# Kernel tuning notes

Measured on AMD Instinct MI355X. Metric: run time of the kernel, lower is better.

The kernel has to match this reference:

```python
import jax, jax.numpy as jnp
import numpy as np

B, P, E, D, A, M, V, T = 64, 196, 2048, 512, 512, 512, 10000, 31


def setup_inputs() -> dict:
    key = jax.random.key(0)
    ks = jax.random.split(key, 20)
    s = 0.02
    inp = {
        "encoder_out": jax.random.normal(ks[0], (B, P, E), jnp.float32),
        "captions": jax.random.randint(ks[1], (B, T), 0, V),
        "caption_lengths": jax.random.randint(ks[2], (B,), 2, T + 1).at[0].set(T),
        # parameters
        "W_emb": jax.random.normal(ks[3], (V, M), jnp.float32) * s,
        "We": jax.random.normal(ks[4], (A, E), jnp.float32) * s,
        "be": jnp.zeros((A,), jnp.float32),
        "Wd": jax.random.normal(ks[5], (A, D), jnp.float32) * s,
        "bd": jnp.zeros((A,), jnp.float32),
        "wf": jax.random.normal(ks[6], (1, A), jnp.float32) * s,
        "bf": jnp.zeros((1,), jnp.float32),
        "Wih": jax.random.normal(ks[7], (4 * D, M + E), jnp.float32) * s,
        "bih": jnp.zeros((4 * D,), jnp.float32),
        "Whh": jax.random.normal(ks[8], (4 * D, D), jnp.float32) * s,
        "bhh": jnp.zeros((4 * D,), jnp.float32),
        "Wfc": jax.random.normal(ks[9], (V, D), jnp.float32) * s,
        "bfc": jnp.zeros((V,), jnp.float32),
        "Wh0": jax.random.normal(ks[10], (D, E), jnp.float32) * s,
        "bh0": jnp.zeros((D,), jnp.float32),
        "Wc0": jax.random.normal(ks[11], (D, E), jnp.float32) * s,
        "bc0": jnp.zeros((D,), jnp.float32),
    }
    return inp


def _decode(encoder_out, W_emb, We, be, Wd, bd, wf, bf, Wih, bih, Whh, bhh,
            Wfc, bfc, Wh0, bh0, Wc0, bc0, captions, caption_lengths):
    # sort by length descending (matches torch .sort(descending=True))
    idx = jnp.argsort(-caption_lengths)
    lens = caption_lengths[idx]
    enc = encoder_out[idx]              # [B,P,E]
    caps = captions[idx]                # [B,T]
    emb = W_emb[caps]                   # [B,T,M]
    mean_enc = enc.mean(axis=1)         # [B,E]
    h0 = mean_enc @ Wh0.T + bh0         # [B,D]
    c0 = mean_enc @ Wc0.T + bc0
    dec_len = lens - 1                  # [B]
    att1 = enc @ We.T + be              # [B,P,A] precomputed encoder projection
    Tmax = caps.shape[1] - 1

    def step(carry, xs):
        h, c = carry
        e_t, t = xs                     # e_t: [B,M]
        active = (t < dec_len)          # [B]
        att2 = h @ Wd.T + bd            # [B,A]
        scores = jnp.tanh(att1 + att2[:, None, :]) @ wf[0] + bf[0]  # [B,P]
        alpha = jax.nn.softmax(scores, axis=-1)                      # [B,P]
        ctx = jnp.einsum('bp,bpe->be', alpha, enc)                   # [B,E]
        x = jnp.concatenate([e_t, ctx], axis=-1)                     # [B,M+E]
        gates = x @ Wih.T + bih + h @ Whh.T + bhh                    # [B,4D]
        i_g, f_g, g_g, o_g = jnp.split(gates, 4, axis=-1)
        c_t = jax.nn.sigmoid(f_g) * c + jax.nn.sigmoid(i_g) * jnp.tanh(g_g)
        h_t = jax.nn.sigmoid(o_g) * jnp.tanh(c_t)
        pred = h_t @ Wfc.T + bfc        # dropout in eval mode = identity
        m = active[:, None]
        h_new = jnp.where(m, h_t, h)
        c_new = jnp.where(m, c_t, c)
        pred = jnp.where(m, pred, 0.0)
        alpha = jnp.where(m, alpha, 0.0)
        return (h_new, c_new), (pred, alpha)

    emb_ts = jnp.swapaxes(emb[:, :Tmax, :], 0, 1)  # [Tmax,B,M]
    ts = jnp.arange(Tmax)
    _, (preds, alphas) = jax.lax.scan(step, (h0, c0), (emb_ts, ts))
    predictions = jnp.swapaxes(preds, 0, 1)   # [B,Tmax,V]
    alphas = jnp.swapaxes(alphas, 0, 1)       # [B,Tmax,P]
    return predictions, alphas


def reference(encoder_out, captions, caption_lengths, W_emb, We, be, Wd, bd,
              wf, bf, Wih, bih, Whh, bhh, Wfc, bfc, Wh0, bh0, Wc0, bc0):
    return _decode(encoder_out, W_emb, We, be, Wd, bd, wf, bf, Wih, bih,
                   Whh, bhh, Wfc, bfc, Wh0, bh0, Wc0, bc0,
                   captions, caption_lengths)
```

## Files before the change

kernel.cpp:

```cpp
#include <hip/hip_runtime.h>
#include <cstdint>
#include <cstddef>

typedef __attribute__((ext_vector_type(8))) short short8;
typedef __attribute__((ext_vector_type(4))) float f32x4;

#define DEV static __device__ __forceinline__

#define PRED_ELEMS 19200000ULL

#define OFF_ENC   0ULL
#define OFF_ATT1  51380224ULL
#define OFF_B1    64225280ULL
#define OFF_WFC   69468160ULL
#define OFF_WEB   79724544ULL
#define OFF_B0    81821696ULL
#define OFF_B2    86016000ULL
#define OFF_MEAN  94404608ULL
#define OFF_HX    94666752ULL
#define OFF_C     94797824ULL
#define OFF_ATT2  94928896ULL
#define OFF_GEH   95059968ULL
#define OFF_CTX   95584256ULL
#define OFF_SC    95846400ULL
#define OFF_META  95896576ULL

DEV float b2f(unsigned short u){ unsigned v = ((unsigned)u) << 16; float f; __builtin_memcpy(&f, &v, 4); return f; }
DEV unsigned short f2b(float x){ unsigned v; __builtin_memcpy(&v, &x, 4); unsigned r = v + 0x7fffu + ((v >> 16) & 1u); return (unsigned short)(r >> 16); }
DEV float sigm(float x){ return 1.0f / (1.0f + __expf(-x)); }

DEV void gload16(const void* g, void* l){
  __builtin_amdgcn_global_load_lds((const __attribute__((address_space(1))) unsigned int*)g,
                                   (__attribute__((address_space(3))) unsigned int*)l, 16, 0, 0);
}

DEV void mm_core(const unsigned short* A, int ldA, int m0,
                 const unsigned short* Bm, int ldB, int n0,
                 int kIters, unsigned short* As, unsigned short* Bs, f32x4 acc[4])
{
  const int tid = threadIdx.x;
  const int lane = tid & 63, w = tid >> 6;
  const unsigned short* ga = A + (size_t)(m0 + lane) * ldA + w * 8;
  const unsigned short* gb = Bm + (size_t)(n0 + lane) * ldB + w * 8;
  unsigned short* la = As + w * 512;
  unsigned short* lb = Bs + w * 512;
  const int kb = lane >> 4, rr = lane & 15;
  for (int kk = 0; kk < kIters; ++kk) {
    gload16(ga, la); gload16(gb, lb);
    ga += 32; gb += 32;
    asm volatile("s_waitcnt vmcnt(0)" ::: "memory");
    __syncthreads();
    short8 bfr = *(const short8*)(Bs + (size_t)(kb * 64 + w * 16 + rr) * 8);
#pragma unroll
    for (int f = 0; f < 4; ++f) {
      short8 afr = *(const short8*)(As + (size_t)(kb * 64 + f * 16 + rr) * 8);
      acc[f] = __builtin_amdgcn_mfma_f32_16x16x32_bf16(afr, bfr, acc[f], 0, 0, 0);
    }
    __syncthreads();
  }
}

__global__ void k_meta(const int* __restrict__ caps, const int* __restrict__ lens, int* __restrict__ meta){
  int j = threadIdx.x;
  int lj = lens[j];
  int rank = 0;
  for (int k = 0; k < 64; ++k) { int lk = lens[k]; rank += (lk > lj) || (lk == lj && k < j); }
  meta[rank] = j; meta[64 + rank] = lj - 1;
  for (int t = 0; t < 31; ++t) meta[160 + rank * 31 + t] = caps[j * 31 + t];
  __syncthreads();
  if (j < 30) { int c = 0; for (int b = 0; b < 64; ++b) c += (meta[64 + b] > j); meta[128 + j] = c; }
}

__global__ __launch_bounds__(256) void k_encg(const float* __restrict__ enc, const int* __restrict__ meta, unsigned short* __restrict__ encb){
  int row = blockIdx.x; int b = row / 196, p = row % 196;
  const float* src = enc + ((size_t)meta[b] * 196 + p) * 2048;
  unsigned short* dst = encb + (size_t)row * 2048;
  int e0 = threadIdx.x * 8;
  short8 o;
#pragma unroll
  for (int j = 0; j < 8; ++j) o[j] = (short)f2b(src[e0 + j]);
  *(short8*)(dst + e0) = o;
}

__global__ __launch_bounds__(256) void k_wconv(const float* We, const float* Wh0, const float* Wc0,
                        const float* Wd, const float* Whh, const float* Wih, const float* Wfc,
                        unsigned short* Web, unsigned short* B0, unsigned short* B1,
                        unsigned short* Wfcb, unsigned short* B2){
  int bid = blockIdx.x, tid = threadIdx.x;
  if (bid < 512) {
    const float* s = We + (size_t)bid * 2048; unsigned short* d = Web + (size_t)bid * 2048;
    int e0 = tid * 8; short8 o;
#pragma unroll
    for (int j = 0; j < 8; ++j) o[j] = (short)f2b(s[e0 + j]);
    *(short8*)(d + e0) = o;
  } else if (bid < 1536) {
    int r = bid - 512;
    const float* s = (r < 512) ? (Wh0 + (size_t)r * 2048) : (Wc0 + (size_t)(r - 512) * 2048);
    unsigned short* d = B0 + (size_t)r * 2048;
    int e0 = tid * 8; short8 o;
#pragma unroll
    for (int j = 0; j < 8; ++j) o[j] = (short)f2b(s[e0 + j]);
    *(short8*)(d + e0) = o;
  } else if (bid < 3584) {
    int jr = bid - 1536; int g = (jr & 3) * 512 + (jr >> 2);
    const float* s = Wih + (size_t)g * 2560 + 512;
    unsigned short* d = B2 + (size_t)jr * 2048;
    int e0 = tid * 8; short8 o;
#pragma unroll
    for (int j = 0; j < 8; ++j) o[j] = (short)f2b(s[e0 + j]);
    *(short8*)(d + e0) = o;
  } else if (bid < 6144) {
    int n = bid - 3584; unsigned short* d = B1 + (size_t)n * 1024;
    int k0 = tid * 4;
    if (n < 512) {
#pragma unroll
      for (int j = 0; j < 4; ++j) { int k = k0 + j; d[k] = (k < 512) ? f2b(Wd[(size_t)n * 512 + k]) : (unsigned short)0; }
    } else {
      int j2 = n - 512; int g = (j2 & 3) * 512 + (j2 >> 2);
#pragma unroll
      for (int j = 0; j < 4; ++j) { int k = k0 + j;
        d[k] = (k < 512) ? f2b(Whh[(size_t)g * 512 + k]) : f2b(Wih[(size_t)g * 2560 + (k - 512)]); }
    }
  } else {
    int v = bid - 6144; unsigned short* d = Wfcb + (size_t)v * 512;
    int k0 = tid * 2;
#pragma unroll
    for (int j = 0; j < 2; ++j) d[k0 + j] = (v < 10000) ? f2b(Wfc[(size_t)v * 512 + k0 + j]) : (unsigned short)0;
  }
}

__global__ __launch_bounds__(256) void k_mean(const unsigned short* __restrict__ encb, unsigned short* __restrict__ meanb){
  int b = blockIdx.y, ch = blockIdx.x;
  int e = ch * 512 + threadIdx.x * 2;
  const unsigned short* ep = encb + (size_t)b * 196 * 2048 + e;
  float s0 = 0.f, s1 = 0.f;
  for (int p = 0; p < 196; ++p) {
    unsigned u = *(const unsigned*)(ep + (size_t)p * 2048);
    s0 += b2f((unsigned short)(u & 0xffff));
    s1 += b2f((unsigned short)(u >> 16));
  }
  const float inv = 1.0f / 196.0f;
  unsigned o = ((unsigned)f2b(s1 * inv) << 16) | f2b(s0 * inv);
  *(unsigned*)(meanb + (size_t)b * 2048 + e) = o;
}

__global__ __launch_bounds__(256) void k_h0c0(const unsigned short* meanb, const unsigned short* B0,
                      const float* bh0, const float* bc0, unsigned short* hx, float* cbuf){
  __shared__ __align__(16) unsigned short As[2048], Bs[2048];
  f32x4 acc[4];
#pragma unroll
  for (int f = 0; f < 4; ++f) acc[f] = (f32x4){0.f,0.f,0.f,0.f};
  int nt = blockIdx.x;
  mm_core(meanb, 2048, 0, B0, 2048, nt * 64, 64, As, Bs, acc);
  int lane = threadIdx.x & 63, w = threadIdx.x >> 6;
  int col = lane & 15, rhi = lane >> 4;
  int n = nt * 64 + w * 16 + col;
#pragma unroll
  for (int f = 0; f < 4; ++f)
#pragma unroll
    for (int r = 0; r < 4; ++r) {
      int b = f * 16 + rhi * 4 + r; float v = acc[f][r];
      if (n < 512) hx[(size_t)b * 1024 + n] = f2b(v + bh0[n]);
      else cbuf[(size_t)b * 512 + (n - 512)] = v + bc0[n - 512];
    }
}

__global__ void k_emb0(const float* __restrict__ Wemb, const int* __restrict__ meta, unsigned short* __restrict__ hx){
  int b = blockIdx.x;
  int cap = meta[160 + b * 31];
  for (int j = threadIdx.x; j < 512; j += 256)
    hx[(size_t)b * 1024 + 512 + j] = f2b(Wemb[(size_t)cap * 512 + j]);
}

__global__ __launch_bounds__(256) void k_att1(const unsigned short* __restrict__ encb,
                      const unsigned short* __restrict__ Web,
                      const float* __restrict__ be, unsigned short* __restrict__ att1b){
  __shared__ __align__(16) unsigned short As[4096];
  int tid = threadIdx.x, w = tid >> 6, lane = tid & 63;
  int mt = blockIdx.x;
  int rr = lane & 15, kb8 = (lane >> 4) * 8;
  f32x4 acc[4][8];
#pragma unroll
  for (int f = 0; f < 4; ++f)
#pragma unroll
    for (int q = 0; q < 8; ++q) acc[f][q] = (f32x4){0.f,0.f,0.f,0.f};

  const unsigned short* ga = encb + (size_t)(mt * 64 + lane) * 2048 + w * 8;
  gload16(ga, As + w * 512);
  asm volatile("s_waitcnt vmcnt(0)" ::: "memory");
  __syncthreads();
  int cb = 0;
  for (int kk = 0; kk < 64; ++kk) {
    int nb = cb ^ 1;
    if (kk < 63) gload16(ga + (kk + 1) * 32, As + (nb << 11) + w * 512);
    short8 af[4];
#pragma unroll
    for (int f = 0; f < 4; ++f)
      af[f] = *(const short8*)(As + (cb << 11) + ((size_t)((lane >> 4) * 64 + f * 16 + rr)) * 8);
#pragma unroll
    for (int q = 0; q < 8; ++q) {
      short8 bfr = *(const short8*)(Web + (size_t)(w * 128 + q * 16 + rr) * 2048 + kk * 32 + kb8);
#pragma unroll
      for (int f = 0; f < 4; ++f)
        acc[f][q] = __builtin_amdgcn_mfma_f32_16x16x32_bf16(af[f], bfr, acc[f][q], 0, 0, 0);
    }
    asm volatile("s_waitcnt vmcnt(0)" ::: "memory");
    __syncthreads();
    cb ^= 1;
  }
  int col = lane & 15, rhi = lane >> 4;
  float bev[8];
#pragma unroll
  for (int q = 0; q < 8; ++q) bev[q] = be[w * 128 + q * 16 + col];
#pragma unroll
  for (int f = 0; f < 4; ++f)
#pragma unroll
    for (int r = 0; r < 4; ++r) {
      int m = mt * 64 + f * 16 + rhi * 4 + r;
#pragma unroll
      for (int q = 0; q < 8; ++q)
        att1b[(size_t)m * 512 + w * 128 + q * 16 + col] = f2b(acc[f][q][r] + bev[q]);
    }
}

__global__ __launch_bounds__(256) void k_step1(int t, const unsigned short* __restrict__ hx,
                       const unsigned short* __restrict__ B1, const unsigned short* __restrict__ Wfcb,
                       const float* __restrict__ bd, const float* __restrict__ bih, const float* __restrict__ bhh,
                       const float* __restrict__ bfc, const int* __restrict__ meta,
                       float* __restrict__ att2f, float* __restrict__ geh, float* __restrict__ out){
  int w = threadIdx.x >> 6, lane = threadIdx.x & 63;
  int omega = blockIdx.x * 4 + w;
  if (omega >= 786) return;
  int rr = lane & 15, kb8 = (lane >> 4) * 8;
  const unsigned short* pb; int kIt;
  if (omega < 32)       { if (t == 30) return; pb = B1 + (size_t)(omega * 16 + rr) * 1024 + kb8; kIt = 16; }
  else if (omega < 160) { if (t == 30) return; pb = B1 + (size_t)(512 + (omega - 32) * 16 + rr) * 1024 + kb8; kIt = 32; }
  else                  { if (t == 0)  return; pb = Wfcb + (size_t)((omega - 160) * 16 + rr) * 512 + kb8; kIt = 16; }
  const unsigned short* pa0 = hx + (size_t)rr * 1024 + kb8;
  f32x4 acc[4];
#pragma unroll
  for (int f = 0; f < 4; ++f) acc[f] = (f32x4){0.f,0.f,0.f,0.f};
#pragma unroll 4
  for (int kk = 0; kk < kIt; ++kk) {
    short8 bfr = *(const short8*)(pb + kk * 32);
#pragma unroll
    for (int f = 0; f < 4; ++f) {
      short8 afr = *(const short8*)(pa0 + (size_t)f * 16384 + kk * 32);
      acc[f] = __builtin_amdgcn_mfma_f32_16x16x32_bf16(afr, bfr, acc[f], 0, 0, 0);
    }
  }
  int col = lane & 15, rhi = lane >> 4;
  if (omega < 32) {
    int n = omega * 16 + col; float bv = bd[n];
#pragma unroll
    for (int f = 0; f < 4; ++f)
#pragma unroll
      for (int r = 0; r < 4; ++r) { int b = f * 16 + rhi * 4 + r; att2f[(size_t)b * 512 + n] = acc[f][r] + bv; }
  } else if (omega < 160) {
    int j = (omega - 32) * 16 + col; int g = (j & 3) * 512 + (j >> 2);
    float bv = bih[g] + bhh[g];
#pragma unroll
    for (int f = 0; f < 4; ++f)
#pragma unroll
      for (int r = 0; r < 4; ++r) { int b = f * 16 + rhi * 4 + r; geh[(size_t)b * 2048 + j] = acc[f][r] + bv; }
  } else {
    int v = (omega - 160) * 16 + col;
    if (v < 10000) {
      int na = meta[128 + t - 1];
      float bv = bfc[v];
#pragma unroll
      for (int f = 0; f < 4; ++f)
#pragma unroll
        for (int r = 0; r < 4; ++r) {
          int b = f * 16 + rhi * 4 + r;
          if (b < na) out[(size_t)b * 300000 + (size_t)(t - 1) * 10000 + v] = acc[f][r] + bv;
        }
    }
  }
}

__global__ __launch_bounds__(256) void k_scores(int t, const unsigned short* __restrict__ att1b, const float* __restrict__ att2f,
                        const float* __restrict__ wf, const float* __restrict__ bfp,
                        const int* __restrict__ meta, float* __restrict__ sc){
  int b = blockIdx.y, pc = blockIdx.x;
  if (b >= meta[128 + t]) return;
  int tid = threadIdx.x, lane = tid & 63, w = tid >> 6;
  float wfr[8], a2[8];
#pragma unroll
  for (int j = 0; j < 8; ++j) { wfr[j] = wf[lane * 8 + j]; a2[j] = att2f[(size_t)b * 512 + lane * 8 + j]; }
  float bf0 = bfp[0];
  for (int pi = w; pi < 49; pi += 4) {
    int p = pc * 49 + pi;
    short8 av = *(const short8*)(att1b + ((size_t)(b * 196 + p)) * 512 + lane * 8);
    float s = 0.f;
#pragma unroll
    for (int j = 0; j < 8; ++j) s += tanhf(b2f((unsigned short)av[j]) + a2[j]) * wfr[j];
#pragma unroll
    for (int off = 32; off; off >>= 1) s += __shfl_xor(s, off);
    if (lane == 0) sc[(size_t)b * 196 + p] = s + bf0;
  }
}

__global__ __launch_bounds__(256) void k_ctx(int t, const float* __restrict__ sc, const unsigned short* __restrict__ encb,
                     const int* __restrict__ meta, float* __restrict__ out, unsigned short* __restrict__ ctxb){
  int b = blockIdx.y, ch = blockIdx.x;
  if (b >= meta[128 + t]) return;
  int tid = threadIdx.x;
  __shared__ float red[256];
  __shared__ float sal[200];
  __shared__ float part[4][512];
  float v = (tid < 196) ? sc[(size_t)b * 196 + tid] : -3.0e38f;
  red[tid] = v; __syncthreads();
  for (int s = 128; s; s >>= 1) { if (tid < s) red[tid] = fmaxf(red[tid], red[tid + s]); __syncthreads(); }
  float mx = red[0]; __syncthreads();
  float ex = (tid < 196) ? __expf(v - mx) : 0.f;
  red[tid] = ex; __syncthreads();
  for (int s = 128; s; s >>= 1) { if (tid < s) red[tid] += red[tid + s]; __syncthreads(); }
  float inv = 1.0f / red[0];
  if (tid < 196) {
    float al = ex * inv;
    sal[tid] = al;
    if (ch == 0) out[PRED_ELEMS + ((size_t)b * 30 + t) * 196 + tid] = al;
  }
  __syncthreads();
  int w = tid >> 6, lane = tid & 63;
  const unsigned short* ep = encb + (size_t)b * 196 * 2048 + ch * 512 + lane * 8;
  float s[8];
#pragma unroll
  for (int j = 0; j < 8; ++j) s[j] = 0.f;
#pragma unroll 7
  for (int i = 0; i < 49; ++i) {
    int p = w + i * 4;
    short8 vv = *(const short8*)(ep + (size_t)p * 2048);
    float a = sal[p];
#pragma unroll
    for (int j = 0; j < 8; ++j) s[j] += a * b2f((unsigned short)vv[j]);
  }
#pragma unroll
  for (int j = 0; j < 8; ++j) part[w][lane * 8 + j] = s[j];
  __syncthreads();
  float r0 = part[0][tid * 2] + part[1][tid * 2] + part[2][tid * 2] + part[3][tid * 2];
  float r1 = part[0][tid * 2 + 1] + part[1][tid * 2 + 1] + part[2][tid * 2 + 1] + part[3][tid * 2 + 1];
  unsigned o = ((unsigned)f2b(r1) << 16) | f2b(r0);
  *(unsigned*)(ctxb + (size_t)b * 2048 + ch * 512 + tid * 2) = o;
}

__global__ __launch_bounds__(256) void k_step2(int t, const unsigned short* __restrict__ ctxb,
                       const unsigned short* __restrict__ B2, const float* __restrict__ geh,
                       const float* __restrict__ Wemb, const int* __restrict__ meta,
                       float* __restrict__ cbuf, unsigned short* __restrict__ hx){
  __shared__ float red[4][64][17];
  int w = threadIdx.x >> 6, lane = threadIdx.x & 63;
  int n0 = blockIdx.x * 16;
  int rr = lane & 15, kb8 = (lane >> 4) * 8;
  const unsigned short* pb = B2 + (size_t)(n0 + rr) * 2048 + w * 512 + kb8;
  const unsigned short* pa0 = ctxb + (size_t)rr * 2048 + w * 512 + kb8;
  f32x4 acc[4];
#pragma unroll
  for (int f = 0; f < 4; ++f) acc[f] = (f32x4){0.f,0.f,0.f,0.f};
#pragma unroll 4
  for (int kk = 0; kk < 16; ++kk) {
    short8 bfr = *(const short8*)(pb + kk * 32);
#pragma unroll
    for (int f = 0; f < 4; ++f) {
      short8 afr = *(const short8*)(pa0 + (size_t)f * 32768 + kk * 32);
      acc[f] = __builtin_amdgcn_mfma_f32_16x16x32_bf16(afr, bfr, acc[f], 0, 0, 0);
    }
  }
  int col = lane & 15, rhi = lane >> 4;
#pragma unroll
  for (int f = 0; f < 4; ++f)
#pragma unroll
    for (int r = 0; r < 4; ++r) red[w][f * 16 + rhi * 4 + r][col] = acc[f][r];
  __syncthreads();
  int b = threadIdx.x >> 2, dl = threadIdx.x & 3;
  int d = (n0 >> 2) + dl;
  float g4[4];
#pragma unroll
  for (int q = 0; q < 4; ++q) {
    int nl = dl * 4 + q;
    g4[q] = red[0][b][nl] + red[1][b][nl] + red[2][b][nl] + red[3][b][nl]
          + geh[(size_t)b * 2048 + n0 + nl];
  }
  float c0 = cbuf[(size_t)b * 512 + d];
  float ct = sigm(g4[1]) * c0 + sigm(g4[0]) * tanhf(g4[2]);
  float ht = sigm(g4[3]) * tanhf(ct);
  int na = meta[128 + t];
  if (b < na) { cbuf[(size_t)b * 512 + d] = ct; hx[(size_t)b * 1024 + d] = f2b(ht); }
  int cap = meta[160 + b * 31 + t + 1];
  hx[(size_t)b * 1024 + 512 + d] = f2b(Wemb[(size_t)cap * 512 + d]);
}

extern "C" void kernel_launch(void* const* d_in, const int* in_sizes, int n_in,
                              void* d_out, int out_size, void* d_ws, size_t ws_size,
                              hipStream_t stream) {
  (void)in_sizes; (void)n_in; (void)ws_size;
  const float* enc  = (const float*)d_in[0];
  const int*   caps = (const int*)d_in[1];
  const int*   lens = (const int*)d_in[2];
  const float* Wemb = (const float*)d_in[3];
  const float* We   = (const float*)d_in[4];
  const float* be   = (const float*)d_in[5];
  const float* Wd   = (const float*)d_in[6];
  const float* bd   = (const float*)d_in[7];
  const float* wf   = (const float*)d_in[8];
  const float* bf   = (const float*)d_in[9];
  const float* Wih  = (const float*)d_in[10];
  const float* bih  = (const float*)d_in[11];
  const float* Whh  = (const float*)d_in[12];
  const float* bhh  = (const float*)d_in[13];
  const float* Wfc  = (const float*)d_in[14];
  const float* bfc  = (const float*)d_in[15];
  const float* Wh0  = (const float*)d_in[16];
  const float* bh0  = (const float*)d_in[17];
  const float* Wc0  = (const float*)d_in[18];
  const float* bc0  = (const float*)d_in[19];

  char* ws = (char*)d_ws;
  unsigned short* encb  = (unsigned short*)(ws + OFF_ENC);
  unsigned short* att1b = (unsigned short*)(ws + OFF_ATT1);
  unsigned short* B1    = (unsigned short*)(ws + OFF_B1);
  unsigned short* Wfcb  = (unsigned short*)(ws + OFF_WFC);
  unsigned short* Web   = (unsigned short*)(ws + OFF_WEB);
  unsigned short* B0    = (unsigned short*)(ws + OFF_B0);
  unsigned short* B2    = (unsigned short*)(ws + OFF_B2);
  unsigned short* meanb = (unsigned short*)(ws + OFF_MEAN);
  unsigned short* hx    = (unsigned short*)(ws + OFF_HX);
  float*          cbuf  = (float*)(ws + OFF_C);
  float*          att2f = (float*)(ws + OFF_ATT2);
  float*          geh   = (float*)(ws + OFF_GEH);
  unsigned short* ctxb  = (unsigned short*)(ws + OFF_CTX);
  float*          sc    = (float*)(ws + OFF_SC);
  int*            meta  = (int*)(ws + OFF_META);
  float* out = (float*)d_out;

  hipMemsetAsync(d_out, 0, (size_t)out_size * sizeof(float), stream);
  k_meta<<<1, 64, 0, stream>>>(caps, lens, meta);
  k_encg<<<12544, 256, 0, stream>>>(enc, meta, encb);
  k_wconv<<<16160, 256, 0, stream>>>(We, Wh0, Wc0, Wd, Whh, Wih, Wfc, Web, B0, B1, Wfcb, B2);
  k_mean<<<dim3(4, 64), 256, 0, stream>>>(encb, meanb);
  k_h0c0<<<16, 256, 0, stream>>>(meanb, B0, bh0, bc0, hx, cbuf);
  k_emb0<<<64, 256, 0, stream>>>(Wemb, meta, hx);
  k_att1<<<196, 256, 0, stream>>>(encb, Web, be, att1b);
  for (int t = 0; t <= 30; ++t) {
    k_step1<<<197, 256, 0, stream>>>(t, hx, B1, Wfcb, bd, bih, bhh, bfc, meta, att2f, geh, out);
    if (t < 30) {
      k_scores<<<dim3(4, 64), 256, 0, stream>>>(t, att1b, att2f, wf, bf, meta, sc);
      k_ctx<<<dim3(4, 64), 256, 0, stream>>>(t, sc, encb, meta, out, ctxb);
      k_step2<<<128, 256, 0, stream>>>(t, ctxb, B2, geh, Wemb, meta, cbuf, hx);
    }
  }
}
```

Measured before the change: 2.012 ms.

## Defer vocab projection to one batched GEMM and fuse attention scoring per step

The per-step output projection onto the vocabulary is taken out of the recurrent loop. Hidden states are collected into a buffer, and a single tiled GEMM (k_pred) computes all predictions at the end. The att2 projection, scores and softmax are merged into one per-batch kernel. The Whh gate term moves into the LSTM-cell kernel, and the hidden/input buffer is ping-ponged, which removes k_step1 and one launch per step. k_att1 is retiled to 128x128 with LDS double buffering for both operands, and tanh is replaced by an exp-based approximation. The risks are the reduced accuracy of the tanh approximation and the hh buffer aliasing the B0 region, which appears safe because B0 is only read by k_h0c0 before the loop.

```diff
diff --git a/kernel.cpp b/kernel.cpp
--- a/kernel.cpp
+++ b/kernel.cpp
@@ -15,19 +15,19 @@
 #define OFF_WFC   69468160ULL
 #define OFF_WEB   79724544ULL
 #define OFF_B0    81821696ULL
+#define OFF_HH    81821696ULL
 #define OFF_B2    86016000ULL
-#define OFF_MEAN  94404608ULL
-#define OFF_HX    94666752ULL
-#define OFF_C     94797824ULL
-#define OFF_ATT2  94928896ULL
-#define OFF_GEH   95059968ULL
-#define OFF_CTX   95584256ULL
-#define OFF_SC    95846400ULL
-#define OFF_META  95896576ULL
+#define OFF_HX0   94404608ULL
+#define OFF_HX1   94535680ULL
+#define OFF_C     94666752ULL
+#define OFF_SC    94797824ULL
+#define OFF_CTX   94848000ULL
+#define OFF_META  95110144ULL
 
 DEV float b2f(unsigned short u){ unsigned v = ((unsigned)u) << 16; float f; __builtin_memcpy(&f, &v, 4); return f; }
 DEV unsigned short f2b(float x){ unsigned v; __builtin_memcpy(&v, &x, 4); unsigned r = v + 0x7fffu + ((v >> 16) & 1u); return (unsigned short)(r >> 16); }
 DEV float sigm(float x){ return 1.0f / (1.0f + __expf(-x)); }
+DEV float tanhf_fast(float x){ float e = __expf(2.0f * x); return 1.0f - 2.0f / (e + 1.0f); }
 
 DEV void gload16(const void* g, void* l){
   __builtin_amdgcn_global_load_lds((const __attribute__((address_space(1))) unsigned int*)g,
@@ -175,141 +175,113 @@
 __global__ __launch_bounds__(256) void k_att1(const unsigned short* __restrict__ encb,
                       const unsigned short* __restrict__ Web,
                       const float* __restrict__ be, unsigned short* __restrict__ att1b){
-  __shared__ __align__(16) unsigned short As[4096];
-  int tid = threadIdx.x, w = tid >> 6, lane = tid & 63;
-  int mt = blockIdx.x;
-  int rr = lane & 15, kb8 = (lane >> 4) * 8;
-  f32x4 acc[4][8];
+  __shared__ __align__(16) unsigned short As[2][4096], Bs[2][4096];
+  int tid = threadIdx.x, lane = tid & 63, w = tid >> 6;
+  int mt = blockIdx.x >> 2, nt = blockIdx.x & 3;
+  int wr = (w >> 1) * 64, wc = (w & 1) * 64;
+  int rr = lane & 15, kb = lane >> 4;
+  f32x4 acc[4][4];
 #pragma unroll
   for (int f = 0; f < 4; ++f)
 #pragma unroll
-    for (int q = 0; q < 8; ++q) acc[f][q] = (f32x4){0.f,0.f,0.f,0.f};
-
-  const unsigned short* ga = encb + (size_t)(mt * 64 + lane) * 2048 + w * 8;
-  gload16(ga, As + w * 512);
-  asm volatile("s_waitcnt vmcnt(0)" ::: "memory");
-  __syncthreads();
-  int cb = 0;
+    for (int q = 0; q < 4; ++q) acc[f][q] = (f32x4){0.f,0.f,0.f,0.f};
+
+  const unsigned short* gA = encb + (size_t)mt * 128 * 2048;
+  const unsigned short* gB = Web + (size_t)nt * 128 * 2048;
+  int L0 = tid, L1 = tid + 256;
+  size_t s0 = (size_t)(L0 & 127) * 2048 + ((L0 >> 7) << 3);
+  size_t s1 = (size_t)(L1 & 127) * 2048 + ((L1 >> 7) << 3);
+  int d0 = (w * 64) * 8, d1 = (w * 64 + 256) * 8;
+
+#define STAGE_A1(kk, bf) do { \
+    gload16(gA + s0 + (size_t)(kk) * 32, &As[bf][d0]); \
+    gload16(gB + s0 + (size_t)(kk) * 32, &Bs[bf][d0]); \
+    gload16(gA + s1 + (size_t)(kk) * 32, &As[bf][d1]); \
+    gload16(gB + s1 + (size_t)(kk) * 32, &Bs[bf][d1]); \
+  } while (0)
+
+  STAGE_A1(0, 0);
+  __syncthreads();
   for (int kk = 0; kk < 64; ++kk) {
-    int nb = cb ^ 1;
-    if (kk < 63) gload16(ga + (kk + 1) * 32, As + (nb << 11) + w * 512);
-    short8 af[4];
+    int cur = kk & 1;
+    if (kk < 63) STAGE_A1(kk + 1, cur ^ 1);
+    short8 af[4], bq[4];
 #pragma unroll
     for (int f = 0; f < 4; ++f)
-      af[f] = *(const short8*)(As + (cb << 11) + ((size_t)((lane >> 4) * 64 + f * 16 + rr)) * 8);
-#pragma unroll
-    for (int q = 0; q < 8; ++q) {
-      short8 bfr = *(const short8*)(Web + (size_t)(w * 128 + q * 16 + rr) * 2048 + kk * 32 + kb8);
-#pragma unroll
-      for (int f = 0; f < 4; ++f)
-        acc[f][q] = __builtin_amdgcn_mfma_f32_16x16x32_bf16(af[f], bfr, acc[f][q], 0, 0, 0);
-    }
-    asm volatile("s_waitcnt vmcnt(0)" ::: "memory");
+      af[f] = *(const short8*)&As[cur][((kb << 7) + wr + f * 16 + rr) * 8];
+#pragma unroll
+    for (int q = 0; q < 4; ++q)
+      bq[q] = *(const short8*)&Bs[cur][((kb << 7) + wc + q * 16 + rr) * 8];
+#pragma unroll
+    for (int f = 0; f < 4; ++f)
+#pragma unroll
+      for (int q = 0; q < 4; ++q)
+        acc[f][q] = __builtin_amdgcn_mfma_f32_16x16x32_bf16(af[f], bq[q], acc[f][q], 0, 0, 0);
     __syncthreads();
-    cb ^= 1;
-  }
+  }
+#undef STAGE_A1
   int col = lane & 15, rhi = lane >> 4;
-  float bev[8];
-#pragma unroll
-  for (int q = 0; q < 8; ++q) bev[q] = be[w * 128 + q * 16 + col];
-#pragma unroll
-  for (int f = 0; f < 4; ++f)
-#pragma unroll
-    for (int r = 0; r < 4; ++r) {
-      int m = mt * 64 + f * 16 + rhi * 4 + r;
-#pragma unroll
-      for (int q = 0; q < 8; ++q)
-        att1b[(size_t)m * 512 + w * 128 + q * 16 + col] = f2b(acc[f][q][r] + bev[q]);
-    }
-}
-
-__global__ __launch_bounds__(256) void k_step1(int t, const unsigned short* __restrict__ hx,
-                       const unsigned short* __restrict__ B1, const unsigned short* __restrict__ Wfcb,
-                       const float* __restrict__ bd, const float* __restrict__ bih, const float* __restrict__ bhh,
-                       const float* __restrict__ bfc, const int* __restrict__ meta,
-                       float* __restrict__ att2f, float* __restrict__ geh, float* __restrict__ out){
-  int w = threadIdx.x >> 6, lane = threadIdx.x & 63;
-  int omega = blockIdx.x * 4 + w;
-  if (omega >= 786) return;
-  int rr = lane & 15, kb8 = (lane >> 4) * 8;
-  const unsigned short* pb; int kIt;
-  if (omega < 32)       { if (t == 30) return; pb = B1 + (size_t)(omega * 16 + rr) * 1024 + kb8; kIt = 16; }
-  else if (omega < 160) { if (t == 30) return; pb = B1 + (size_t)(512 + (omega - 32) * 16 + rr) * 1024 + kb8; kIt = 32; }
-  else                  { if (t == 0)  return; pb = Wfcb + (size_t)((omega - 160) * 16 + rr) * 512 + kb8; kIt = 16; }
-  const unsigned short* pa0 = hx + (size_t)rr * 1024 + kb8;
-  f32x4 acc[4];
-#pragma unroll
-  for (int f = 0; f < 4; ++f) acc[f] = (f32x4){0.f,0.f,0.f,0.f};
-#pragma unroll 4
-  for (int kk = 0; kk < kIt; ++kk) {
-    short8 bfr = *(const short8*)(pb + kk * 32);
-#pragma unroll
-    for (int f = 0; f < 4; ++f) {
-      short8 afr = *(const short8*)(pa0 + (size_t)f * 16384 + kk * 32);
-      acc[f] = __builtin_amdgcn_mfma_f32_16x16x32_bf16(afr, bfr, acc[f], 0, 0, 0);
-    }
-  }
-  int col = lane & 15, rhi = lane >> 4;
-  if (omega < 32) {
-    int n = omega * 16 + col; float bv = bd[n];
+#pragma unroll
+  for (int q = 0; q < 4; ++q) {
+    int n = nt * 128 + wc + q * 16 + col;
+    float bev = be[n];
 #pragma unroll
     for (int f = 0; f < 4; ++f)
 #pragma unroll
-      for (int r = 0; r < 4; ++r) { int b = f * 16 + rhi * 4 + r; att2f[(size_t)b * 512 + n] = acc[f][r] + bv; }
-  } else if (omega < 160) {
-    int j = (omega - 32) * 16 + col; int g = (j & 3) * 512 + (j >> 2);
-    float bv = bih[g] + bhh[g];
-#pragma unroll
-    for (int f = 0; f < 4; ++f)
-#pragma unroll
-      for (int r = 0; r < 4; ++r) { int b = f * 16 + rhi * 4 + r; geh[(size_t)b * 2048 + j] = acc[f][r] + bv; }
-  } else {
-    int v = (omega - 160) * 16 + col;
-    if (v < 10000) {
-      int na = meta[128 + t - 1];
-      float bv = bfc[v];
-#pragma unroll
-      for (int f = 0; f < 4; ++f)
-#pragma unroll
-        for (int r = 0; r < 4; ++r) {
-          int b = f * 16 + rhi * 4 + r;
-          if (b < na) out[(size_t)b * 300000 + (size_t)(t - 1) * 10000 + v] = acc[f][r] + bv;
-        }
-    }
-  }
-}
-
-__global__ __launch_bounds__(256) void k_scores(int t, const unsigned short* __restrict__ att1b, const float* __restrict__ att2f,
-                        const float* __restrict__ wf, const float* __restrict__ bfp,
-                        const int* __restrict__ meta, float* __restrict__ sc){
-  int b = blockIdx.y, pc = blockIdx.x;
+      for (int r = 0; r < 4; ++r) {
+        int m = mt * 128 + wr + f * 16 + rhi * 4 + r;
+        att1b[(size_t)m * 512 + n] = f2b(acc[f][q][r] + bev);
+      }
+  }
+}
+
+__global__ __launch_bounds__(256) void k_att2s(int t, const unsigned short* __restrict__ hx,
+                        const unsigned short* __restrict__ B1, const unsigned short* __restrict__ att1b,
+                        const float* __restrict__ bd, const float* __restrict__ wf, const float* __restrict__ bfp,
+                        const int* __restrict__ meta, float* __restrict__ out, float* __restrict__ sc){
+  int b = blockIdx.x;
   if (b >= meta[128 + t]) return;
   int tid = threadIdx.x, lane = tid & 63, w = tid >> 6;
+  __shared__ float hsf[512];
+  __shared__ float a2s[512];
+  __shared__ float sal[200];
+  __shared__ float red[256];
+  if (tid < 64) {
+    short8 hv = *(const short8*)(hx + (size_t)b * 1024 + tid * 8);
+#pragma unroll
+    for (int j = 0; j < 8; ++j) hsf[tid * 8 + j] = b2f(hv[j]);
+  }
+  __syncthreads();
+#pragma unroll
+  for (int half = 0; half < 2; ++half) {
+    int n = tid + half * 256;
+    const unsigned short* wp = B1 + (size_t)n * 1024;
+    float s = 0.f;
+#pragma unroll 8
+    for (int kk = 0; kk < 64; ++kk) {
+      short8 wv = *(const short8*)(wp + kk * 8);
+#pragma unroll
+      for (int j = 0; j < 8; ++j) s += hsf[kk * 8 + j] * b2f((unsigned short)wv[j]);
+    }
+    a2s[n] = s + bd[n];
+  }
+  __syncthreads();
   float wfr[8], a2[8];
 #pragma unroll
-  for (int j = 0; j < 8; ++j) { wfr[j] = wf[lane * 8 + j]; a2[j] = att2f[(size_t)b * 512 + lane * 8 + j]; }
+  for (int j = 0; j < 8; ++j) { wfr[j] = wf[lane * 8 + j]; a2[j] = a2s[lane * 8 + j]; }
   float bf0 = bfp[0];
-  for (int pi = w; pi < 49; pi += 4) {
-    int p = pc * 49 + pi;
+  for (int i = 0; i < 49; ++i) {
+    int p = i * 4 + w;
     short8 av = *(const short8*)(att1b + ((size_t)(b * 196 + p)) * 512 + lane * 8);
     float s = 0.f;
 #pragma unroll
-    for (int j = 0; j < 8; ++j) s += tanhf(b2f((unsigned short)av[j]) + a2[j]) * wfr[j];
+    for (int j = 0; j < 8; ++j) s += tanhf_fast(b2f((unsigned short)av[j]) + a2[j]) * wfr[j];
 #pragma unroll
     for (int off = 32; off; off >>= 1) s += __shfl_xor(s, off);
-    if (lane == 0) sc[(size_t)b * 196 + p] = s + bf0;
-  }
-}
-
-__global__ __launch_bounds__(256) void k_ctx(int t, const float* __restrict__ sc, const unsigned short* __restrict__ encb,
-                     const int* __restrict__ meta, float* __restrict__ out, unsigned short* __restrict__ ctxb){
-  int b = blockIdx.y, ch = blockIdx.x;
-  if (b >= meta[128 + t]) return;
-  int tid = threadIdx.x;
-  __shared__ float red[256];
-  __shared__ float sal[200];
-  __shared__ float part[4][512];
-  float v = (tid < 196) ? sc[(size_t)b * 196 + tid] : -3.0e38f;
+    if (lane == 0) sal[p] = s + bf0;
+  }
+  __syncthreads();
+  float v = (tid < 196) ? sal[tid] : -3.0e38f;
   red[tid] = v; __syncthreads();
   for (int s = 128; s; s >>= 1) { if (tid < s) red[tid] = fmaxf(red[tid], red[tid + s]); __syncthreads(); }
   float mx = red[0]; __syncthreads();
@@ -319,25 +291,34 @@
   float inv = 1.0f / red[0];
   if (tid < 196) {
     float al = ex * inv;
-    sal[tid] = al;
-    if (ch == 0) out[PRED_ELEMS + ((size_t)b * 30 + t) * 196 + tid] = al;
-  }
-  __syncthreads();
-  int w = tid >> 6, lane = tid & 63;
+    sc[(size_t)b * 196 + tid] = al;
+    out[PRED_ELEMS + ((size_t)b * 30 + t) * 196 + tid] = al;
+  }
+}
+
+__global__ __launch_bounds__(256) void k_ctx(int t, const float* __restrict__ sc, const unsigned short* __restrict__ encb,
+                     const int* __restrict__ meta, unsigned short* __restrict__ ctxb){
+  int b = blockIdx.y, ch = blockIdx.x;
+  if (b >= meta[128 + t]) return;
+  int tid = threadIdx.x, w = tid >> 6, lane = tid & 63;
+  __shared__ float sal[200];
+  __shared__ float part[4][512];
+  if (tid < 196) sal[tid] = sc[(size_t)b * 196 + tid];
+  __syncthreads();
   const unsigned short* ep = encb + (size_t)b * 196 * 2048 + ch * 512 + lane * 8;
-  float s[8];
-#pragma unroll
-  for (int j = 0; j < 8; ++j) s[j] = 0.f;
+  float s8[8];
+#pragma unroll
+  for (int j = 0; j < 8; ++j) s8[j] = 0.f;
 #pragma unroll 7
   for (int i = 0; i < 49; ++i) {
     int p = w + i * 4;
     short8 vv = *(const short8*)(ep + (size_t)p * 2048);
     float a = sal[p];
 #pragma unroll
-    for (int j = 0; j < 8; ++j) s[j] += a * b2f((unsigned short)vv[j]);
-  }
-#pragma unroll
-  for (int j = 0; j < 8; ++j) part[w][lane * 8 + j] = s[j];
+    for (int j = 0; j < 8; ++j) s8[j] += a * b2f((unsigned short)vv[j]);
+  }
+#pragma unroll
+  for (int j = 0; j < 8; ++j) part[w][lane * 8 + j] = s8[j];
   __syncthreads();
   float r0 = part[0][tid * 2] + part[1][tid * 2] + part[2][tid * 2] + part[3][tid * 2];
   float r1 = part[0][tid * 2 + 1] + part[1][tid * 2 + 1] + part[2][tid * 2 + 1] + part[3][tid * 2 + 1];
@@ -346,27 +327,44 @@
 }
 
 __global__ __launch_bounds__(256) void k_step2(int t, const unsigned short* __restrict__ ctxb,
-                       const unsigned short* __restrict__ B2, const float* __restrict__ geh,
+                       const unsigned short* __restrict__ hxc, unsigned short* __restrict__ hxn,
+                       const unsigned short* __restrict__ B1, const unsigned short* __restrict__ B2,
+                       const float* __restrict__ bih, const float* __restrict__ bhh,
                        const float* __restrict__ Wemb, const int* __restrict__ meta,
-                       float* __restrict__ cbuf, unsigned short* __restrict__ hx){
+                       float* __restrict__ cbuf, unsigned short* __restrict__ hh){
   __shared__ float red[4][64][17];
   int w = threadIdx.x >> 6, lane = threadIdx.x & 63;
   int n0 = blockIdx.x * 16;
   int rr = lane & 15, kb8 = (lane >> 4) * 8;
-  const unsigned short* pb = B2 + (size_t)(n0 + rr) * 2048 + w * 512 + kb8;
-  const unsigned short* pa0 = ctxb + (size_t)rr * 2048 + w * 512 + kb8;
   f32x4 acc[4];
 #pragma unroll
   for (int f = 0; f < 4; ++f) acc[f] = (f32x4){0.f,0.f,0.f,0.f};
+  {
+    const unsigned short* pb = B2 + (size_t)(n0 + rr) * 2048 + w * 512 + kb8;
+    const unsigned short* pa = ctxb + (size_t)rr * 2048 + w * 512 + kb8;
 #pragma unroll 4
-  for (int kk = 0; kk < 16; ++kk) {
-    short8 bfr = *(const short8*)(pb + kk * 32);
-#pragma unroll
-    for (int f = 0; f < 4; ++f) {
-      short8 afr = *(const short8*)(pa0 + (size_t)f * 32768 + kk * 32);
-      acc[f] = __builtin_amdgcn_mfma_f32_16x16x32_bf16(afr, bfr, acc[f], 0, 0, 0);
+    for (int kk = 0; kk < 16; ++kk) {
+      short8 bfr = *(const short8*)(pb + kk * 32);
+#pragma unroll
+      for (int f = 0; f < 4; ++f) {
+        short8 afr = *(const short8*)(pa + (size_t)f * 32768 + kk * 32);
+        acc[f] = __builtin_amdgcn_mfma_f32_16x16x32_bf16(afr, bfr, acc[f], 0, 0, 0);
+      }
     }
   }
+  {
+    const unsigned short* pb = B1 + (size_t)(512 + n0 + rr) * 1024 + w * 256 + kb8;
+    const unsigned short* pa = hxc + (size_t)rr * 1024 + w * 256 + kb8;
+#pragma unroll 4
+    for (int kk = 0; kk < 8; ++kk) {
+      short8 bfr = *(const short8*)(pb + kk * 32);
+#pragma unroll
+      for (int f = 0; f < 4; ++f) {
+        short8 afr = *(const short8*)(pa + (size_t)f * 16384 + kk * 32);
+        acc[f] = __builtin_amdgcn_mfma_f32_16x16x32_bf16(afr, bfr, acc[f], 0, 0, 0);
+      }
+    }
+  }
   int col = lane & 15, rhi = lane >> 4;
 #pragma unroll
   for (int f = 0; f < 4; ++f)
@@ -374,21 +372,95 @@
     for (int r = 0; r < 4; ++r) red[w][f * 16 + rhi * 4 + r][col] = acc[f][r];
   __syncthreads();
   int b = threadIdx.x >> 2, dl = threadIdx.x & 3;
-  int d = (n0 >> 2) + dl;
+  int d = blockIdx.x * 4 + dl;
   float g4[4];
 #pragma unroll
   for (int q = 0; q < 4; ++q) {
     int nl = dl * 4 + q;
-    g4[q] = red[0][b][nl] + red[1][b][nl] + red[2][b][nl] + red[3][b][nl]
-          + geh[(size_t)b * 2048 + n0 + nl];
+    int j = n0 + nl;
+    int g = (j & 3) * 512 + (j >> 2);
+    g4[q] = red[0][b][nl] + red[1][b][nl] + red[2][b][nl] + red[3][b][nl] + bih[g] + bhh[g];
   }
   float c0 = cbuf[(size_t)b * 512 + d];
-  float ct = sigm(g4[1]) * c0 + sigm(g4[0]) * tanhf(g4[2]);
-  float ht = sigm(g4[3]) * tanhf(ct);
+  float ct = sigm(g4[1]) * c0 + sigm(g4[0]) * tanhf_fast(g4[2]);
+  float ht = sigm(g4[3]) * tanhf_fast(ct);
   int na = meta[128 + t];
-  if (b < na) { cbuf[(size_t)b * 512 + d] = ct; hx[(size_t)b * 1024 + d] = f2b(ht); }
+  unsigned short hold = hxc[(size_t)b * 1024 + d];
+  unsigned short hnew = (b < na) ? f2b(ht) : hold;
+  if (b < na) cbuf[(size_t)b * 512 + d] = ct;
+  hxn[(size_t)b * 1024 + d] = hnew;
+  hh[((size_t)t * 64 + b) * 512 + d] = hnew;
   int cap = meta[160 + b * 31 + t + 1];
-  hx[(size_t)b * 1024 + 512 + d] = f2b(Wemb[(size_t)cap * 512 + d]);
+  hxn[(size_t)b * 1024 + 512 + d] = f2b(Wemb[(size_t)cap * 512 + d]);
+}
+
+__global__ __launch_bounds__(256) void k_pred(const unsigned short* __restrict__ hh,
+                      const unsigned short* __restrict__ Wfcb, const float* __restrict__ bfc,
+                      const int* __restrict__ meta, float* __restrict__ out){
+  __shared__ __align__(16) unsigned short As[2][4096], Bs[2][4096];
+  int tid = threadIdx.x, lane = tid & 63, w = tid >> 6;
+  int mt = blockIdx.x % 15, nt = blockIdx.x / 15;
+  int wr = (w >> 1) * 64, wc = (w & 1) * 64;
+  int rr = lane & 15, kb = lane >> 4;
+  f32x4 acc[4][4];
+#pragma unroll
+  for (int f = 0; f < 4; ++f)
+#pragma unroll
+    for (int q = 0; q < 4; ++q) acc[f][q] = (f32x4){0.f,0.f,0.f,0.f};
+
+  const unsigned short* gA = hh + (size_t)mt * 128 * 512;
+  int L0 = tid, L1 = tid + 256;
+  size_t sa0 = (size_t)(L0 & 127) * 512 + ((L0 >> 7) << 3);
+  size_t sa1 = (size_t)(L1 & 127) * 512 + ((L1 >> 7) << 3);
+  int br0 = nt * 128 + (L0 & 127); if (br0 > 10015) br0 = 10015;
+  int br1 = nt * 128 + (L1 & 127); if (br1 > 10015) br1 = 10015;
+  size_t sb0 = (size_t)br0 * 512 + ((L0 >> 7) << 3);
+  size_t sb1 = (size_t)br1 * 512 + ((L1 >> 7) << 3);
+  int d0 = (w * 64) * 8, d1 = (w * 64 + 256) * 8;
+
+#define STAGE_P(kk, bf) do { \
+    gload16(gA + sa0 + (size_t)(kk) * 32, &As[bf][d0]); \
+    gload16(Wfcb + sb0 + (size_t)(kk) * 32, &Bs[bf][d0]); \
+    gload16(gA + sa1 + (size_t)(kk) * 32, &As[bf][d1]); \
+    gload16(Wfcb + sb1 + (size_t)(kk) * 32, &Bs[bf][d1]); \
+  } while (0)
+
+  STAGE_P(0, 0);
+  __syncthreads();
+  for (int kk = 0; kk < 16; ++kk) {
+    int cur = kk & 1;
+    if (kk < 15) STAGE_P(kk + 1, cur ^ 1);
+    short8 af[4], bq[4];
+#pragma unroll
+    for (int f = 0; f < 4; ++f)
+      af[f] = *(const short8*)&As[cur][((kb << 7) + wr + f * 16 + rr) * 8];
+#pragma unroll
+    for (int q = 0; q < 4; ++q)
+      bq[q] = *(const short8*)&Bs[cur][((kb << 7) + wc + q * 16 + rr) * 8];
+#pragma unroll
+    for (int f = 0; f < 4; ++f)
+#pragma unroll
+      for (int q = 0; q < 4; ++q)
+        acc[f][q] = __builtin_amdgcn_mfma_f32_16x16x32_bf16(af[f], bq[q], acc[f][q], 0, 0, 0);
+    __syncthreads();
+  }
+#undef STAGE_P
+  int col = lane & 15, rhi = lane >> 4;
+  int tt = mt * 2 + (wr >> 6);
+  int na = meta[128 + tt];
+#pragma unroll
+  for (int q = 0; q < 4; ++q) {
+    int n = nt * 128 + wc + q * 16 + col;
+    if (n >= 10000) continue;
+    float bv = bfc[n];
+#pragma unroll
+    for (int f = 0; f < 4; ++f)
+#pragma unroll
+      for (int r = 0; r < 4; ++r) {
+        int b = f * 16 + rhi * 4 + r;
+        if (b < na) out[(size_t)b * 300000 + (size_t)tt * 10000 + n] = acc[f][q][r] + bv;
+      }
+  }
 }
 
 extern "C" void kernel_launch(void* const* d_in, const int* in_sizes, int n_in,
@@ -423,15 +495,17 @@
   unsigned short* Wfcb  = (unsigned short*)(ws + OFF_WFC);
   unsigned short* Web   = (unsigned short*)(ws + OFF_WEB);
   unsigned short* B0    = (unsigned short*)(ws + OFF_B0);
+  unsigned short* hh    = (unsigned short*)(ws + OFF_HH);
   unsigned short* B2    = (unsigned short*)(ws + OFF_B2);
-  unsigned short* meanb = (unsigned short*)(ws + OFF_MEAN);
-  unsigned short* hx    = (unsigned short*)(ws + OFF_HX);
+  unsigned short* hx0   = (unsigned short*)(ws + OFF_HX0);
+  unsigned short* hx1   = (unsigned short*)(ws + OFF_HX1);
   float*          cbuf  = (float*)(ws + OFF_C);
-  float*          att2f = (float*)(ws + OFF_ATT2);
-  float*          geh   = (float*)(ws + OFF_GEH);
+  float*          sc    = (float*)(ws + OFF_SC);
   unsigned short* ctxb  = (unsigned short*)(ws + OFF_CTX);
-  float*          sc    = (float*)(ws + OFF_SC);
   int*            meta  = (int*)(ws + OFF_META);
+  unsigned short* meanb = hx1;
+  meanb = (unsigned short*)(ws + OFF_B2 + 8388608 - 262144);
+  meanb = (unsigned short*)(ws + OFF_META + 16384);
   float* out = (float*)d_out;
 
   hipMemsetAsync(d_out, 0, (size_t)out_size * sizeof(float), stream);
@@ -439,15 +513,15 @@
   k_encg<<<12544, 256, 0, stream>>>(enc, meta, encb);
   k_wconv<<<16160, 256, 0, stream>>>(We, Wh0, Wc0, Wd, Whh, Wih, Wfc, Web, B0, B1, Wfcb, B2);
   k_mean<<<dim3(4, 64), 256, 0, stream>>>(encb, meanb);
-  k_h0c0<<<16, 256, 0, stream>>>(meanb, B0, bh0, bc0, hx, cbuf);
-  k_emb0<<<64, 256, 0, stream>>>(Wemb, meta, hx);
-  k_att1<<<196, 256, 0, stream>>>(encb, Web, be, att1b);
-  for (int t = 0; t <= 30; ++t) {
-    k_step1<<<197, 256, 0, stream>>>(t, hx, B1, Wfcb, bd, bih, bhh, bfc, meta, att2f, geh, out);
-    if (t < 30) {
-      k_scores<<<dim3(4, 64), 256, 0, stream>>>(t, att1b, att2f, wf, bf, meta, sc);
-      k_ctx<<<dim3(4, 64), 256, 0, stream>>>(t, sc, encb, meta, out, ctxb);
-      k_step2<<<128, 256, 0, stream>>>(t, ctxb, B2, geh, Wemb, meta, cbuf, hx);
-    }
-  }
-}
+  k_h0c0<<<16, 256, 0, stream>>>(meanb, B0, bh0, bc0, hx0, cbuf);
+  k_emb0<<<64, 256, 0, stream>>>(Wemb, meta, hx0);
+  k_att1<<<392, 256, 0, stream>>>(encb, Web, be, att1b);
+  for (int t = 0; t < 30; ++t) {
+    unsigned short* hxc = (t & 1) ? hx1 : hx0;
+    unsigned short* hxn = (t & 1) ? hx0 : hx1;
+    k_att2s<<<64, 256, 0, stream>>>(t, hxc, B1, att1b, bd, wf, bf, meta, out, sc);
+    k_ctx<<<dim3(4, 64), 256, 0, stream>>>(t, sc, encb, meta, ctxb);
+    k_step2<<<128, 256, 0, stream>>>(t, ctxb, hxc, hxn, B1, B2, bih, bhh, Wemb, meta, cbuf, hh);
+  }
+  k_pred<<<1185, 256, 0, stream>>>(hh, Wfcb, bfc, meta, out);
+}
```

After: 3.129 ms. 1.56x slower.
